# Performance work log

Measured on AMD Instinct MI355X. Metric: run time of the kernel, lower is better.

Reference implementation:

```python
import jax, jax.numpy as jnp
import numpy as np
from jax import lax

EPS = 1e-5

def rmsnorm(x, w, eps=EPS):
    x = jnp.clip(x, -100.0, 100.0)
    var = jnp.clip(jnp.mean(x * x, axis=-1, keepdims=True), eps, None)
    x = jnp.clip(x * lax.rsqrt(var + eps), -10.0, 10.0)
    return w * x

def activation_quant(x):
    x = jnp.clip(x, -50.0, 50.0)
    max_val = jnp.clip(jnp.max(jnp.abs(x), axis=-1, keepdims=True), 0.0001, None)
    scale = 127.0 / max_val
    return jnp.clip(jnp.round(x * scale), -128, 127) / scale

def weight_quant(w):
    scale = jnp.clip(jnp.mean(jnp.abs(w)), 1e-8, None)
    return jnp.sign(w - jnp.mean(w)) * scale

def bitlinear(x, w, norm_w):
    # x: [T, in], w: [out, in], norm_w: [in]
    xn = rmsnorm(x, norm_w)
    xq = xn + lax.stop_gradient(activation_quant(xn) - xn)
    wq = w + lax.stop_gradient(weight_quant(w) - w)
    return jnp.einsum('ti,oi->to', xq, wq)

def expert_fwd(x, wg, wu, wd, n_g, n_u, n_d):
    gate = jnp.clip(bitlinear(x, wg, n_g), -20.0, 20.0)
    up = bitlinear(x, wu, n_u)
    hidden = jnp.clip(jax.nn.silu(gate) * up, -1000.0, 1000.0)
    return bitlinear(hidden, wd, n_d)

def setup_inputs() -> dict:
    key = jax.random.key(0)
    B, S, H, I, E = 4, 2048, 768, 2048, 8
    ks = jax.random.split(key, 12)
    std_h = 0.02 / np.sqrt(H)
    std_i = 0.02 / np.sqrt(I)
    return {
        'hidden_states': jax.random.normal(ks[0], (B, S, H), jnp.float32),
        'router_w': 0.01 * jax.random.normal(ks[1], (E, H), jnp.float32),
        'router_b': jnp.zeros((E,), jnp.float32),
        'Wg': std_h * jax.random.normal(ks[2], (E, I, H), jnp.float32),
        'Wu': std_h * jax.random.normal(ks[3], (E, I, H), jnp.float32),
        'Wd': std_i * jax.random.normal(ks[4], (E, H, I), jnp.float32),
        'ng': jnp.ones((E, H), jnp.float32),
        'nu': jnp.ones((E, H), jnp.float32),
        'nd': jnp.ones((E, I), jnp.float32),
        'sWg': std_h * jax.random.normal(ks[5], (I, H), jnp.float32),
        'sWu': std_h * jax.random.normal(ks[6], (I, H), jnp.float32),
        'sWd': std_i * jax.random.normal(ks[7], (H, I), jnp.float32),
        'sng': jnp.ones((H,), jnp.float32),
        'snu': jnp.ones((H,), jnp.float32),
        'snd': jnp.ones((I,), jnp.float32),
    }

def reference(hidden_states, router_w, router_b, Wg, Wu, Wd, ng, nu, nd, sWg, sWu, sWd, sng, snu, snd):
    B, S, H = hidden_states.shape
    E = router_w.shape[0]
    K = 2  # num_experts_per_tok
    x = hidden_states.reshape(-1, H)  # [T, H]
    router_logits = jnp.einsum('th,eh->te', x, router_w) + router_b  # [T, E]
    routing_weights = jax.nn.softmax(router_logits, axis=-1)
    top_w, top_idx = lax.top_k(routing_weights, K)  # [T, K]
    top_w = top_w / (jnp.sum(top_w, axis=-1, keepdims=True) + 1e-8)
    out = jnp.zeros_like(x)
    for e in range(E):
        w_e = jnp.sum(jnp.where(top_idx == e, top_w, 0.0), axis=-1)  # [T]
        y_e = expert_fwd(x, Wg[e], Wu[e], Wd[e], ng[e], nu[e], nd[e])
        out = out + y_e * w_e[:, None]
    out = out + expert_fwd(x, sWg, sWu, sWd, sng, snu, snd)
    out = jnp.clip(out, -10000.0, 10000.0)
    return out.reshape(B, S, H), router_logits
```

## Files before the change

kernel.cpp:

```cpp
#include <hip/hip_runtime.h>
#include <hip/hip_bf16.h>
#include <math.h>

#define TOK 8192
#define HD 768
#define ID 2048
#define NE 8
#define MSIZE (2048*768)
#define BM 128
#define BK 64
#define R_SHARED 8192
#define R_MAX 25600

typedef int v4i __attribute__((ext_vector_type(4)));
typedef __attribute__((address_space(1))) void gas_void;
typedef __attribute__((address_space(3))) void las_void;

__device__ __forceinline__ void g2lds16(const void* g, void* l) {
  __builtin_amdgcn_global_load_lds((gas_void*)g, (las_void*)l, 16, 0, 0);
}

__device__ __forceinline__ float clipf(float v, float lo, float hi) {
  return fminf(fmaxf(v, lo), hi);
}

__device__ __forceinline__ float wred_sum(float v) {
#pragma unroll
  for (int o = 32; o > 0; o >>= 1) v += __shfl_down(v, o, 64);
  return v;
}
__device__ __forceinline__ float wred_max(float v) {
#pragma unroll
  for (int o = 32; o > 0; o >>= 1) v = fmaxf(v, __shfl_down(v, o, 64));
  return v;
}

__device__ __forceinline__ const float* matsel(int mat, const float* Wg, const float* Wu,
                                               const float* Wd, const float* sWg,
                                               const float* sWu, const float* sWd) {
  if (mat < 8)  return Wg + (size_t)mat * MSIZE;
  if (mat < 16) return Wu + (size_t)(mat - 8) * MSIZE;
  if (mat < 24) return Wd + (size_t)(mat - 16) * MSIZE;
  if (mat == 24) return sWg;
  if (mat == 25) return sWu;
  return sWd;
}

__global__ __launch_bounds__(256)
void k_wstats(const float* __restrict__ Wg, const float* __restrict__ Wu,
              const float* __restrict__ Wd, const float* __restrict__ sWg,
              const float* __restrict__ sWu, const float* __restrict__ sWd,
              double* __restrict__ stats) {
  int mat = blockIdx.y;
  const float* p = matsel(mat, Wg, Wu, Wd, sWg, sWu, sWd);
  int tid = threadIdx.x;
  double s = 0.0, sa = 0.0;
  for (size_t i = (size_t)blockIdx.x * 256 + tid; i < (size_t)MSIZE;
       i += (size_t)gridDim.x * 256) {
    double v = (double)p[i];
    s += v; sa += fabs(v);
  }
  __shared__ double rs[256], ra[256];
  rs[tid] = s; ra[tid] = sa; __syncthreads();
  for (int st = 128; st > 0; st >>= 1) {
    if (tid < st) { rs[tid] += rs[tid + st]; ra[tid] += ra[tid + st]; }
    __syncthreads();
  }
  if (tid == 0) {
    atomicAdd(&stats[mat * 2 + 0], rs[0]);
    atomicAdd(&stats[mat * 2 + 1], ra[0]);
  }
}

__global__ void k_wfinal(const double* __restrict__ stats, double* __restrict__ wmean,
                         float* __restrict__ wscale) {
  int m = threadIdx.x;
  if (m < 27) {
    wmean[m] = stats[m * 2] / (double)MSIZE;
    double sc = stats[m * 2 + 1] / (double)MSIZE;
    wscale[m] = (float)fmax(sc, 1e-8);
  }
}

__global__ __launch_bounds__(256)
void k_wquant(const float* __restrict__ Wg, const float* __restrict__ Wu,
              const float* __restrict__ Wd, const float* __restrict__ sWg,
              const float* __restrict__ sWu, const float* __restrict__ sWd,
              const double* __restrict__ wmean, signed char* __restrict__ tw) {
  int mat = blockIdx.y;
  const float* p = matsel(mat, Wg, Wu, Wd, sWg, sWu, sWd);
  const float4* p4 = (const float4*)p;
  int* t4 = (int*)(tw + (size_t)mat * MSIZE);
  double mu = wmean[mat];
  for (int i = blockIdx.x * 256 + threadIdx.x; i < MSIZE / 4; i += gridDim.x * 256) {
    float4 v = p4[i];
    int b0 = ((double)v.x > mu) ? 1 : (((double)v.x < mu) ? -1 : 0);
    int b1 = ((double)v.y > mu) ? 1 : (((double)v.y < mu) ? -1 : 0);
    int b2 = ((double)v.z > mu) ? 1 : (((double)v.z < mu) ? -1 : 0);
    int b3 = ((double)v.w > mu) ? 1 : (((double)v.w < mu) ? -1 : 0);
    t4[i] = (b0 & 255) | ((b1 & 255) << 8) | ((b2 & 255) << 16) | ((b3 & 255) << 24);
  }
}

__global__ __launch_bounds__(256)
void k_router(const float* __restrict__ x, const float* __restrict__ rw,
              const float* __restrict__ rb, float* __restrict__ logits,
              int* __restrict__ top_idx, float* __restrict__ top_w) {
  int wv = threadIdx.x >> 6, ln = threadIdx.x & 63;
  int t = blockIdx.x * 4 + wv;
  const float4* xr = (const float4*)(x + (size_t)t * HD);
  const float4* rw4 = (const float4*)rw;
  float acc[NE] = {};
#pragma unroll
  for (int i = 0; i < 3; ++i) {
    float4 xv = xr[ln + i * 64];
#pragma unroll
    for (int e = 0; e < NE; ++e) {
      float4 w4 = rw4[e * 192 + ln + i * 64];
      acc[e] += xv.x * w4.x + xv.y * w4.y + xv.z * w4.z + xv.w * w4.w;
    }
  }
#pragma unroll
  for (int e = 0; e < NE; ++e) acc[e] = wred_sum(acc[e]);
  if (ln == 0) {
    float lg[NE], m = -1e30f;
#pragma unroll
    for (int e = 0; e < NE; ++e) {
      lg[e] = acc[e] + rb[e];
      logits[(size_t)t * NE + e] = lg[e];
      m = fmaxf(m, lg[e]);
    }
    float p[NE], s = 0.f;
#pragma unroll
    for (int e = 0; e < NE; ++e) { p[e] = expf(lg[e] - m); s += p[e]; }
    float inv = 1.f / s;
#pragma unroll
    for (int e = 0; e < NE; ++e) p[e] *= inv;
    int e1 = 0; float b1 = p[0];
    for (int e = 1; e < NE; ++e) if (p[e] > b1) { b1 = p[e]; e1 = e; }
    int e2 = -1; float b2 = -1.f;
    for (int e = 0; e < NE; ++e) if (e != e1 && p[e] > b2) { b2 = p[e]; e2 = e; }
    float sw = b1 + b2 + 1e-8f;
    top_idx[t * 2 + 0] = e1; top_idx[t * 2 + 1] = e2;
    top_w[t * 2 + 0] = b1 / sw; top_w[t * 2 + 1] = b2 / sw;
  }
}

__global__ __launch_bounds__(1024)
void k_hist(const int* __restrict__ top_idx, int* __restrict__ counts) {
  __shared__ int h[NE];
  if (threadIdx.x < NE) h[threadIdx.x] = 0;
  __syncthreads();
  for (int i = threadIdx.x; i < TOK * 2; i += 1024) atomicAdd(&h[top_idx[i]], 1);
  __syncthreads();
  if (threadIdx.x < NE) counts[threadIdx.x] = h[threadIdx.x];
}

__global__ void k_initrows(int* __restrict__ rows_token, float* __restrict__ rows_w,
                           int* __restrict__ rows_expert) {
  int r = blockIdx.x * blockDim.x + threadIdx.x;
  if (r >= R_MAX) return;
  if (r < R_SHARED) { rows_token[r] = r; rows_w[r] = 1.f; rows_expert[r] = NE; }
  else { rows_token[r] = -1; rows_w[r] = 0.f; rows_expert[r] = 0; }
}

__global__ void k_offsets(const int* __restrict__ counts, int* __restrict__ offs,
                          int* __restrict__ fill) {
  if (threadIdx.x == 0) {
    int off = R_SHARED;
    for (int e = 0; e < NE; ++e) {
      offs[e] = off;
      off += ((counts[e] + BM - 1) / BM) * BM;
    }
    offs[NE] = off;
  }
  if (threadIdx.x < NE) fill[threadIdx.x] = 0;
}

__global__ __launch_bounds__(256)
void k_scatter(const int* __restrict__ top_idx, const float* __restrict__ top_w,
               const int* __restrict__ offs, int* __restrict__ fill,
               int* __restrict__ rows_token, float* __restrict__ rows_w,
               int* __restrict__ rows_expert, int* __restrict__ inv_row) {
  int t = blockIdx.x * 256 + threadIdx.x;
  int ln = threadIdx.x & 63;
  unsigned long long lt = (ln == 63) ? 0x7fffffffffffffffull
                                     : ((1ull << ln) - 1);
#pragma unroll
  for (int k = 0; k < 2; ++k) {
    int e = top_idx[t * 2 + k];
    unsigned long long peers = 0;
#pragma unroll
    for (int ee = 0; ee < NE; ++ee) {
      unsigned long long m = __ballot(e == ee);
      if (e == ee) peers = m;
    }
    int lead = __ffsll(peers) - 1;
    int rank = __popcll(peers & lt);
    int base = 0;
    if (ln == lead) base = atomicAdd(&fill[e], __popcll(peers));
    base = __shfl(base, lead, 64);
    int r = offs[e] + base + rank;
    rows_token[r] = t;
    rows_w[r] = top_w[t * 2 + k];
    rows_expert[r] = e;
    inv_row[t * 2 + k] = r;
  }
}

__global__ __launch_bounds__(256)
void k_actquant(const float* __restrict__ x, const int* __restrict__ rows_token,
                const int* __restrict__ rows_expert, const float* __restrict__ ng,
                const float* __restrict__ nu, const float* __restrict__ sng,
                const float* __restrict__ snu, signed char* __restrict__ xqg,
                signed char* __restrict__ xqu, float* __restrict__ invg,
                float* __restrict__ invu) {
  int r = blockIdx.x, tid = threadIdx.x;
  int wv = tid >> 6, ln = tid & 63;
  int tok = rows_token[r];
  if (tok < 0) {
    if (tid < 192) {
      ((int*)(xqg + (size_t)r * HD))[tid] = 0;
      ((int*)(xqu + (size_t)r * HD))[tid] = 0;
    }
    if (tid == 0) { invg[r] = 0.f; invu[r] = 0.f; }
    return;
  }
  int e = rows_expert[r];
  const float* wg = (e < NE) ? ng + (size_t)e * HD : sng;
  const float* wu = (e < NE) ? nu + (size_t)e * HD : snu;
  __shared__ float red[3][4];
  float xv[3]; float ss = 0.f;
#pragma unroll
  for (int i = 0; i < 3; ++i) {
    float v = x[(size_t)tok * HD + tid + i * 256];
    v = clipf(v, -100.f, 100.f);
    xv[i] = v; ss += v * v;
  }
  ss = wred_sum(ss);
  if (ln == 0) red[0][wv] = ss;
  __syncthreads();
  float var = fmaxf((red[0][0] + red[0][1] + red[0][2] + red[0][3]) / (float)HD, 1e-5f);
  float rinv = rsqrtf(var + 1e-5f);
  float xng[3], xnu[3]; float ag = 0.f, au = 0.f;
#pragma unroll
  for (int i = 0; i < 3; ++i) {
    float base = clipf(xv[i] * rinv, -10.f, 10.f);
    float tg = clipf(base * wg[tid + i * 256], -50.f, 50.f);
    float tu = clipf(base * wu[tid + i * 256], -50.f, 50.f);
    xng[i] = tg; ag = fmaxf(ag, fabsf(tg));
    xnu[i] = tu; au = fmaxf(au, fabsf(tu));
  }
  ag = wred_max(ag); au = wred_max(au);
  if (ln == 0) { red[1][wv] = ag; red[2][wv] = au; }
  __syncthreads();
  float mg = fmaxf(fmaxf(fmaxf(red[1][0], red[1][1]), fmaxf(red[1][2], red[1][3])), 1e-4f);
  float mu = fmaxf(fmaxf(fmaxf(red[2][0], red[2][1]), fmaxf(red[2][2], red[2][3])), 1e-4f);
  float scg = 127.f / mg, scu = 127.f / mu;
#pragma unroll
  for (int i = 0; i < 3; ++i) {
    xqg[(size_t)r * HD + tid + i * 256] = (signed char)(int)clipf(rintf(xng[i] * scg), -128.f, 127.f);
    xqu[(size_t)r * HD + tid + i * 256] = (signed char)(int)clipf(rintf(xnu[i] * scu), -128.f, 127.f);
  }
  if (tid == 0) { invg[r] = 1.f / scg; invu[r] = 1.f / scu; }
}

__global__ __launch_bounds__(512, 4)
void k_gemm_gu(const signed char* __restrict__ xqg, const signed char* __restrict__ xqu,
               const signed char* __restrict__ tw, const float* __restrict__ wscale,
               const float* __restrict__ invg, const float* __restrict__ invu,
               const int* __restrict__ rows_expert, const int* __restrict__ offs,
               __hip_bfloat16* __restrict__ hidden) {
  int n0 = blockIdx.x * BM;
  int row0 = blockIdx.y * BM;
  if (row0 >= offs[NE]) return;
  int e = rows_expert[row0];
  int mg = (e < NE) ? e : 24;
  int mu = (e < NE) ? e + 8 : 25;
  const signed char* wgp = tw + (size_t)mg * MSIZE;
  const signed char* wup = tw + (size_t)mu * MSIZE;
  __shared__ __align__(16) signed char Ag[2 * BM * BK];
  __shared__ __align__(16) signed char Au[2 * BM * BK];
  __shared__ __align__(16) signed char Bg[2 * BM * BK];
  __shared__ __align__(16) signed char Bu[2 * BM * BK];
  __shared__ float sg[BM], su[BM];
  int tid = threadIdx.x, wv = tid >> 6, ln = tid & 63;
  if (tid < BM) { sg[tid] = invg[row0 + tid]; su[tid] = invu[row0 + tid]; }
  v4i accg[4][2] = {};
  v4i accu[4][2] = {};
  int srow = tid >> 2;
  int swz = (((tid & 3) ^ ((srow >> 1) & 3)) << 4);
  const signed char* pag = xqg + (size_t)(row0 + srow) * HD + swz;
  const signed char* pau = xqu + (size_t)(row0 + srow) * HD + swz;
  const signed char* pbg = wgp + (size_t)(n0 + srow) * HD + swz;
  const signed char* pbu = wup + (size_t)(n0 + srow) * HD + swz;
  int cob = wv * 1024;
  int wm = (wv & 1) * 64, wn = (wv >> 1) * 32;
  int fm = ln & 15;
  int slot16 = (((ln >> 4) ^ ((fm >> 1) & 3)) << 4);
  int offA[4], offB[2];
#pragma unroll
  for (int i = 0; i < 4; ++i) offA[i] = (wm + i * 16 + fm) * BK + slot16;
#pragma unroll
  for (int j = 0; j < 2; ++j) offB[j] = (wn + j * 16 + fm) * BK + slot16;

  auto stage = [&](int buf) {
    int co = buf * 8192 + cob;
    g2lds16(pag, &Ag[co]);
    g2lds16(pau, &Au[co]);
    g2lds16(pbg, &Bg[co]);
    g2lds16(pbu, &Bu[co]);
    pag += BK; pau += BK; pbg += BK; pbu += BK;
  };
  auto compute = [&](int buf) {
    int lb = buf * 8192;
    v4i ar[4], ur[4];
#pragma unroll
    for (int i = 0; i < 4; ++i) {
      ar[i] = *(const v4i*)&Ag[lb + offA[i]];
      ur[i] = *(const v4i*)&Au[lb + offA[i]];
    }
#pragma unroll
    for (int j = 0; j < 2; ++j) {
      v4i bg = *(const v4i*)&Bg[lb + offB[j]];
      v4i bu = *(const v4i*)&Bu[lb + offB[j]];
#pragma unroll
      for (int i = 0; i < 4; ++i) {
        accg[i][j] = __builtin_amdgcn_mfma_i32_16x16x64_i8(ar[i], bg, accg[i][j], 0, 0, 0);
        accu[i][j] = __builtin_amdgcn_mfma_i32_16x16x64_i8(ur[i], bu, accu[i][j], 0, 0, 0);
      }
    }
  };

  const int NIT = HD / BK;
  stage(0);
#pragma unroll 1
  for (int it = 0; it < NIT; it += 2) {
    __syncthreads();
    if (it + 1 < NIT) stage(1);
    compute(0);
    __syncthreads();
    if (it + 2 < NIT) stage(0);
    compute(1);
  }

  float gs = wscale[mg], us = wscale[mu];
  int dq = (ln >> 4) * 4, dn = ln & 15;
#pragma unroll
  for (int i = 0; i < 4; ++i) {
#pragma unroll
    for (int rg = 0; rg < 4; ++rg) {
      int lrow = wm + i * 16 + dq + rg;
      int grow = row0 + lrow;
      float ig = gs * sg[lrow];
      float iu = us * su[lrow];
#pragma unroll
      for (int j = 0; j < 2; ++j) {
        int gcol = n0 + wn + j * 16 + dn;
        float g = (float)accg[i][j][rg] * ig;
        g = clipf(g, -20.f, 20.f);
        float sil = g * __builtin_amdgcn_rcpf(1.f + __expf(-g));
        float u = (float)accu[i][j][rg] * iu;
        float h = clipf(sil * u, -1000.f, 1000.f);
        hidden[(size_t)grow * ID + gcol] = __float2bfloat16(h);
      }
    }
  }
}

__global__ __launch_bounds__(256)
void k_hquant(const __hip_bfloat16* __restrict__ hidden, const int* __restrict__ rows_token,
              const int* __restrict__ rows_expert, const float* __restrict__ nd,
              const float* __restrict__ snd, signed char* __restrict__ hq,
              float* __restrict__ invh) {
  int r = blockIdx.x, tid = threadIdx.x;
  int wv = tid >> 6, ln = tid & 63;
  int tok = rows_token[r];
  if (tok < 0) {
    ((unsigned long long*)(hq + (size_t)r * ID))[tid] = 0ull;
    if (tid == 0) invh[r] = 0.f;
    return;
  }
  int e = rows_expert[r];
  const float2* wn2 = (const float2*)((e < NE) ? nd + (size_t)e * ID : snd);
  const unsigned int* h2 = (const unsigned int*)(hidden + (size_t)r * ID);
  __shared__ float red[2][4];
  float xa[4], xb[4]; float ss = 0.f;
#pragma unroll
  for (int i = 0; i < 4; ++i) {
    unsigned int u = h2[tid + i * 256];
    float a = __uint_as_float(u << 16);
    float b = __uint_as_float(u & 0xffff0000u);
    a = clipf(a, -100.f, 100.f); b = clipf(b, -100.f, 100.f);
    xa[i] = a; xb[i] = b; ss += a * a + b * b;
  }
  ss = wred_sum(ss);
  if (ln == 0) red[0][wv] = ss;
  __syncthreads();
  float var = fmaxf((red[0][0] + red[0][1] + red[0][2] + red[0][3]) / (float)ID, 1e-5f);
  float rinv = rsqrtf(var + 1e-5f);
  float na[4], nb[4]; float amax = 0.f;
#pragma unroll
  for (int i = 0; i < 4; ++i) {
    float2 w = wn2[tid + i * 256];
    float ta = clipf(clipf(xa[i] * rinv, -10.f, 10.f) * w.x, -50.f, 50.f);
    float tb = clipf(clipf(xb[i] * rinv, -10.f, 10.f) * w.y, -50.f, 50.f);
    na[i] = ta; nb[i] = tb;
    amax = fmaxf(amax, fmaxf(fabsf(ta), fabsf(tb)));
  }
  amax = wred_max(amax);
  if (ln == 0) red[1][wv] = amax;
  __syncthreads();
  float mx = fmaxf(fmaxf(fmaxf(red[1][0], red[1][1]), fmaxf(red[1][2], red[1][3])), 1e-4f);
  float sc = 127.f / mx;
  unsigned short* hqs = (unsigned short*)(hq + (size_t)r * ID);
#pragma unroll
  for (int i = 0; i < 4; ++i) {
    int qa = (int)clipf(rintf(na[i] * sc), -128.f, 127.f);
    int qb = (int)clipf(rintf(nb[i] * sc), -128.f, 127.f);
    hqs[tid + i * 256] = (unsigned short)((qa & 255) | ((qb & 255) << 8));
  }
  if (tid == 0) invh[r] = 1.f / sc;
}

__global__ __launch_bounds__(512, 4)
void k_gemm_down(const signed char* __restrict__ hq, const signed char* __restrict__ tw,
                 const float* __restrict__ wscale, const float* __restrict__ invh,
                 const float* __restrict__ rows_w, const int* __restrict__ rows_expert,
                 const int* __restrict__ offs, float* __restrict__ y) {
  int n0 = blockIdx.x * BM;
  int row0 = blockIdx.y * BM;
  if (row0 >= offs[NE]) return;
  int e = rows_expert[row0];
  int md = (e < NE) ? 16 + e : 26;
  const signed char* wdp = tw + (size_t)md * MSIZE;
  __shared__ __align__(16) signed char As[2 * BM * BK];
  __shared__ __align__(16) signed char Bs[2 * BM * BK];
  __shared__ float s_f[BM];
  int tid = threadIdx.x, wv = tid >> 6, ln = tid & 63;
  if (tid < BM) s_f[tid] = invh[row0 + tid] * rows_w[row0 + tid];
  v4i acc[4][2] = {};
  int srow = tid >> 2;
  int swz = (((tid & 3) ^ ((srow >> 1) & 3)) << 4);
  const signed char* pa = hq + (size_t)(row0 + srow) * ID + swz;
  const signed char* pb = wdp + (size_t)(n0 + srow) * ID + swz;
  int cob = wv * 1024;
  int wm = (wv & 1) * 64, wn = (wv >> 1) * 32;
  int fm = ln & 15;
  int slot16 = (((ln >> 4) ^ ((fm >> 1) & 3)) << 4);
  int offA[4], offB[2];
#pragma unroll
  for (int i = 0; i < 4; ++i) offA[i] = (wm + i * 16 + fm) * BK + slot16;
#pragma unroll
  for (int j = 0; j < 2; ++j) offB[j] = (wn + j * 16 + fm) * BK + slot16;

  auto stage = [&](int buf) {
    int co = buf * 8192 + cob;
    g2lds16(pa, &As[co]);
    g2lds16(pb, &Bs[co]);
    pa += BK; pb += BK;
  };
  auto compute = [&](int buf) {
    int lb = buf * 8192;
    v4i a[4];
#pragma unroll
    for (int i = 0; i < 4; ++i) a[i] = *(const v4i*)&As[lb + offA[i]];
#pragma unroll
    for (int j = 0; j < 2; ++j) {
      v4i b = *(const v4i*)&Bs[lb + offB[j]];
#pragma unroll
      for (int i = 0; i < 4; ++i)
        acc[i][j] = __builtin_amdgcn_mfma_i32_16x16x64_i8(a[i], b, acc[i][j], 0, 0, 0);
    }
  };

  const int NIT = ID / BK;
  stage(0);
#pragma unroll 1
  for (int it = 0; it < NIT; it += 2) {
    __syncthreads();
    if (it + 1 < NIT) stage(1);
    compute(0);
    __syncthreads();
    if (it + 2 < NIT) stage(0);
    compute(1);
  }

  float ds = wscale[md];
  int dq = (ln >> 4) * 4, dn = ln & 15;
#pragma unroll
  for (int i = 0; i < 4; ++i) {
#pragma unroll
    for (int rg = 0; rg < 4; ++rg) {
      int lrow = wm + i * 16 + dq + rg;
      float f = ds * s_f[lrow];
#pragma unroll
      for (int j = 0; j < 2; ++j) {
        int gcol = n0 + wn + j * 16 + dn;
        y[(size_t)(row0 + lrow) * HD + gcol] = (float)acc[i][j][rg] * f;
      }
    }
  }
}

__global__ __launch_bounds__(192)
void k_gather(const float* __restrict__ y, const int* __restrict__ inv_row,
              float* __restrict__ out) {
  int t = blockIdx.x, c = threadIdx.x;
  int r1 = inv_row[t * 2 + 0], r2 = inv_row[t * 2 + 1];
  const float4* y4 = (const float4*)y;
  float4 a = y4[(size_t)t * 192 + c];
  float4 b = y4[(size_t)r1 * 192 + c];
  float4 d = y4[(size_t)r2 * 192 + c];
  float4 o;
  o.x = clipf(a.x + b.x + d.x, -10000.f, 10000.f);
  o.y = clipf(a.y + b.y + d.y, -10000.f, 10000.f);
  o.z = clipf(a.z + b.z + d.z, -10000.f, 10000.f);
  o.w = clipf(a.w + b.w + d.w, -10000.f, 10000.f);
  ((float4*)out)[(size_t)t * 192 + c] = o;
}

extern "C" void kernel_launch(void* const* d_in, const int* in_sizes, int n_in,
                              void* d_out, int out_size, void* d_ws, size_t ws_size,
                              hipStream_t stream) {
  (void)in_sizes; (void)n_in; (void)out_size; (void)ws_size;
  const float* x   = (const float*)d_in[0];
  const float* rw  = (const float*)d_in[1];
  const float* rb  = (const float*)d_in[2];
  const float* Wg  = (const float*)d_in[3];
  const float* Wu  = (const float*)d_in[4];
  const float* Wd  = (const float*)d_in[5];
  const float* ng  = (const float*)d_in[6];
  const float* nu  = (const float*)d_in[7];
  const float* nd  = (const float*)d_in[8];
  const float* sWg = (const float*)d_in[9];
  const float* sWu = (const float*)d_in[10];
  const float* sWd = (const float*)d_in[11];
  const float* sng = (const float*)d_in[12];
  const float* snu = (const float*)d_in[13];
  const float* snd = (const float*)d_in[14];
  float* out = (float*)d_out;
  float* logits = out + (size_t)TOK * HD;

  char* ws = (char*)d_ws;
  size_t off = 0;
  auto alloc = [&](size_t b) { size_t o = off; off = (off + b + 255) & ~(size_t)255; return o; };
  signed char* tw   = (signed char*)(ws + alloc((size_t)27 * MSIZE));
  double* stats     = (double*)(ws + alloc(27 * 2 * sizeof(double)));
  double* wmean     = (double*)(ws + alloc(27 * sizeof(double)));
  float* wscale     = (float*)(ws + alloc(27 * sizeof(float)));
  int* counts       = (int*)(ws + alloc(8 * sizeof(int)));
  int* fill         = (int*)(ws + alloc(8 * sizeof(int)));
  int* offs         = (int*)(ws + alloc(16 * sizeof(int)));
  int* top_idx      = (int*)(ws + alloc((size_t)TOK * 2 * sizeof(int)));
  float* top_w      = (float*)(ws + alloc((size_t)TOK * 2 * sizeof(float)));
  int* inv_row      = (int*)(ws + alloc((size_t)TOK * 2 * sizeof(int)));
  int* rows_token   = (int*)(ws + alloc((size_t)R_MAX * sizeof(int)));
  float* rows_w     = (float*)(ws + alloc((size_t)R_MAX * sizeof(float)));
  int* rows_expert  = (int*)(ws + alloc((size_t)R_MAX * sizeof(int)));
  float* invg       = (float*)(ws + alloc((size_t)R_MAX * sizeof(float)));
  float* invu       = (float*)(ws + alloc((size_t)R_MAX * sizeof(float)));
  float* invh       = (float*)(ws + alloc((size_t)R_MAX * sizeof(float)));
  signed char* hq   = (signed char*)(ws + alloc((size_t)R_MAX * ID));
  signed char* xqg  = hq;
  signed char* xqu  = hq + (size_t)R_MAX * HD;
  char* hid_region  = ws + alloc((size_t)R_MAX * ID * 2);
  __hip_bfloat16* hidden = (__hip_bfloat16*)hid_region;
  float* y          = (float*)hid_region;

  hipMemsetAsync(stats, 0, 27 * 2 * sizeof(double), stream);

  k_wstats<<<dim3(64, 27), 256, 0, stream>>>(Wg, Wu, Wd, sWg, sWu, sWd, stats);
  k_wfinal<<<1, 32, 0, stream>>>(stats, wmean, wscale);
  k_wquant<<<dim3(256, 27), 256, 0, stream>>>(Wg, Wu, Wd, sWg, sWu, sWd, wmean, tw);
  k_router<<<TOK / 4, 256, 0, stream>>>(x, rw, rb, logits, top_idx, top_w);
  k_hist<<<1, 1024, 0, stream>>>(top_idx, counts);
  k_initrows<<<(R_MAX + 255) / 256, 256, 0, stream>>>(rows_token, rows_w, rows_expert);
  k_offsets<<<1, 64, 0, stream>>>(counts, offs, fill);
  k_scatter<<<TOK / 256, 256, 0, stream>>>(top_idx, top_w, offs, fill, rows_token,
                                           rows_w, rows_expert, inv_row);
  k_actquant<<<R_MAX, 256, 0, stream>>>(x, rows_token, rows_expert, ng, nu, sng, snu,
                                        xqg, xqu, invg, invu);
  k_gemm_gu<<<dim3(ID / BM, R_MAX / BM), 512, 0, stream>>>(xqg, xqu, tw, wscale, invg, invu,
                                                           rows_expert, offs, hidden);
  k_hquant<<<R_MAX, 256, 0, stream>>>(hidden, rows_token, rows_expert, nd, snd, hq, invh);
  k_gemm_down<<<dim3(HD / BM, R_MAX / BM), 512, 0, stream>>>(hq, tw, wscale, invh,
                                                             rows_w, rows_expert, offs, y);
  k_gather<<<TOK, 192, 0, stream>>>(y, inv_row, out);
}
```

Before: 598.7 us.

## Split gate/up GEMM and switch to 32x32x32 MFMA with direct-global B loads

Replaces the fused gate+up GEMM with two separate kernels sharing a new gemm_core that uses 32x32x32 int8 MFMA, 256-thread blocks, and loads the weight (B) operand directly from global memory into registers instead of staging it through LDS. The gate kernel writes clipped gate values as bf16 into the hidden buffer, and the up kernel reads them back to apply SiLU and the product. The down GEMM is moved onto the same core. This cuts LDS footprint and instruction count per MFMA, but adds an extra bf16 write and read of the full hidden buffer plus uncoalesced, unstaged global B loads.

Measured after the change: 770.5 us. 28.7% more time.

```diff
diff --git a/kernel.cpp b/kernel.cpp
--- a/kernel.cpp
+++ b/kernel.cpp
@@ -13,6 +13,7 @@
 #define R_MAX 25600
 
 typedef int v4i __attribute__((ext_vector_type(4)));
+typedef int v16i __attribute__((ext_vector_type(16)));
 typedef __attribute__((address_space(1))) void gas_void;
 typedef __attribute__((address_space(3))) void las_void;
 
@@ -265,107 +266,135 @@
   if (tid == 0) { invg[r] = 1.f / scg; invu[r] = 1.f / scu; }
 }
 
-__global__ __launch_bounds__(512, 4)
-void k_gemm_gu(const signed char* __restrict__ xqg, const signed char* __restrict__ xqu,
-               const signed char* __restrict__ tw, const float* __restrict__ wscale,
-               const float* __restrict__ invg, const float* __restrict__ invu,
-               const int* __restrict__ rows_expert, const int* __restrict__ offs,
-               __hip_bfloat16* __restrict__ hidden) {
-  int n0 = blockIdx.x * BM;
-  int row0 = blockIdx.y * BM;
+__device__ __forceinline__ void gemm_core(const signed char* __restrict__ aq,
+                                          const signed char* __restrict__ bp,
+                                          int row0, int n0, int kdim, int nit,
+                                          signed char* As, v16i acc[2][2]) {
+  int tid = threadIdx.x, wv = tid >> 6, ln = tid & 63;
+  int lr = ln & 31, lh = ln >> 5;
+  const signed char* pa[2];
+#pragma unroll
+  for (int j = 0; j < 2; ++j)
+    pa[j] = aq + (size_t)(row0 + wv * 32 + lr) * kdim + j * 32 + lh * 16;
+  const signed char* pb[2];
+#pragma unroll
+  for (int j = 0; j < 2; ++j)
+    pb[j] = bp + (size_t)(n0 + (wv >> 1) * 64 + j * 32 + lr) * kdim + lh * 16;
+  int offA[2][2];
+#pragma unroll
+  for (int i = 0; i < 2; ++i)
+#pragma unroll
+    for (int kc = 0; kc < 2; ++kc)
+      offA[i][kc] = ((((wv & 1) * 2 + i) * 2 + kc) << 10) + ln * 16;
+
+  auto stage = [&](int buf) {
+#pragma unroll
+    for (int j = 0; j < 2; ++j) {
+      g2lds16(pa[j], As + buf * 8192 + ((wv * 2 + j) << 10));
+      pa[j] += BK;
+    }
+  };
+  auto compute = [&](int buf) {
+    v4i b[2][2];
+#pragma unroll
+    for (int j = 0; j < 2; ++j) {
+      b[j][0] = *(const v4i*)(pb[j]);
+      b[j][1] = *(const v4i*)(pb[j] + 32);
+      pb[j] += BK;
+    }
+    v4i a[2][2];
+#pragma unroll
+    for (int i = 0; i < 2; ++i)
+#pragma unroll
+      for (int kc = 0; kc < 2; ++kc)
+        a[i][kc] = *(const v4i*)(As + buf * 8192 + offA[i][kc]);
+#pragma unroll
+    for (int kc = 0; kc < 2; ++kc)
+#pragma unroll
+      for (int i = 0; i < 2; ++i)
+#pragma unroll
+        for (int j = 0; j < 2; ++j)
+          acc[i][j] = __builtin_amdgcn_mfma_i32_32x32x32_i8(a[i][kc], b[j][kc], acc[i][j], 0, 0, 0);
+  };
+
+  stage(0);
+#pragma unroll 1
+  for (int it = 0; it < nit; it += 2) {
+    __syncthreads();
+    if (it + 1 < nit) stage(1);
+    compute(0);
+    __syncthreads();
+    if (it + 2 < nit) stage(0);
+    compute(1);
+  }
+}
+
+
+__global__ __launch_bounds__(256, 3)
+void k_gemm_gate(const signed char* __restrict__ xq, const signed char* __restrict__ tw,
+                 const float* __restrict__ wscale, const float* __restrict__ invx,
+                 const int* __restrict__ rows_expert, const int* __restrict__ offs,
+                 __hip_bfloat16* __restrict__ gbuf) {
+  int n0 = blockIdx.x * BM, row0 = blockIdx.y * BM;
   if (row0 >= offs[NE]) return;
   int e = rows_expert[row0];
   int mg = (e < NE) ? e : 24;
+  __shared__ __align__(16) signed char As[2 * 8192];
+  __shared__ float sx[BM];
+  if (threadIdx.x < BM) sx[threadIdx.x] = invx[row0 + threadIdx.x];
+  v16i acc[2][2] = {};
+  gemm_core(xq, tw + (size_t)mg * MSIZE, row0, n0, HD, HD / BK, As, acc);
+  float ws = wscale[mg];
+  int wv = threadIdx.x >> 6, ln = threadIdx.x & 63;
+  int wm = (wv & 1) * 64, wn = (wv >> 1) * 64;
+  int lr = ln & 31, lh = ln >> 5;
+#pragma unroll
+  for (int i = 0; i < 2; ++i)
+#pragma unroll
+    for (int j = 0; j < 2; ++j)
+#pragma unroll
+      for (int r = 0; r < 16; ++r) {
+        int row = wm + i * 32 + (r & 3) + 8 * (r >> 2) + 4 * lh;
+        int col = n0 + wn + j * 32 + lr;
+        float g = (float)acc[i][j][r] * ws * sx[row];
+        g = clipf(g, -20.f, 20.f);
+        gbuf[(size_t)(row0 + row) * ID + col] = __float2bfloat16(g);
+      }
+}
+
+__global__ __launch_bounds__(256, 3)
+void k_gemm_up(const signed char* __restrict__ xq, const signed char* __restrict__ tw,
+               const float* __restrict__ wscale, const float* __restrict__ invx,
+               const int* __restrict__ rows_expert, const int* __restrict__ offs,
+               __hip_bfloat16* __restrict__ gbuf) {
+  int n0 = blockIdx.x * BM, row0 = blockIdx.y * BM;
+  if (row0 >= offs[NE]) return;
+  int e = rows_expert[row0];
   int mu = (e < NE) ? e + 8 : 25;
-  const signed char* wgp = tw + (size_t)mg * MSIZE;
-  const signed char* wup = tw + (size_t)mu * MSIZE;
-  __shared__ __align__(16) signed char Ag[2 * BM * BK];
-  __shared__ __align__(16) signed char Au[2 * BM * BK];
-  __shared__ __align__(16) signed char Bg[2 * BM * BK];
-  __shared__ __align__(16) signed char Bu[2 * BM * BK];
-  __shared__ float sg[BM], su[BM];
-  int tid = threadIdx.x, wv = tid >> 6, ln = tid & 63;
-  if (tid < BM) { sg[tid] = invg[row0 + tid]; su[tid] = invu[row0 + tid]; }
-  v4i accg[4][2] = {};
-  v4i accu[4][2] = {};
-  int srow = tid >> 2;
-  int swz = (((tid & 3) ^ ((srow >> 1) & 3)) << 4);
-  const signed char* pag = xqg + (size_t)(row0 + srow) * HD + swz;
-  const signed char* pau = xqu + (size_t)(row0 + srow) * HD + swz;
-  const signed char* pbg = wgp + (size_t)(n0 + srow) * HD + swz;
-  const signed char* pbu = wup + (size_t)(n0 + srow) * HD + swz;
-  int cob = wv * 1024;
-  int wm = (wv & 1) * 64, wn = (wv >> 1) * 32;
-  int fm = ln & 15;
-  int slot16 = (((ln >> 4) ^ ((fm >> 1) & 3)) << 4);
-  int offA[4], offB[2];
-#pragma unroll
-  for (int i = 0; i < 4; ++i) offA[i] = (wm + i * 16 + fm) * BK + slot16;
-#pragma unroll
-  for (int j = 0; j < 2; ++j) offB[j] = (wn + j * 16 + fm) * BK + slot16;
-
-  auto stage = [&](int buf) {
-    int co = buf * 8192 + cob;
-    g2lds16(pag, &Ag[co]);
-    g2lds16(pau, &Au[co]);
-    g2lds16(pbg, &Bg[co]);
-    g2lds16(pbu, &Bu[co]);
-    pag += BK; pau += BK; pbg += BK; pbu += BK;
-  };
-  auto compute = [&](int buf) {
-    int lb = buf * 8192;
-    v4i ar[4], ur[4];
-#pragma unroll
-    for (int i = 0; i < 4; ++i) {
-      ar[i] = *(const v4i*)&Ag[lb + offA[i]];
-      ur[i] = *(const v4i*)&Au[lb + offA[i]];
-    }
-#pragma unroll
-    for (int j = 0; j < 2; ++j) {
-      v4i bg = *(const v4i*)&Bg[lb + offB[j]];
-      v4i bu = *(const v4i*)&Bu[lb + offB[j]];
-#pragma unroll
-      for (int i = 0; i < 4; ++i) {
-        accg[i][j] = __builtin_amdgcn_mfma_i32_16x16x64_i8(ar[i], bg, accg[i][j], 0, 0, 0);
-        accu[i][j] = __builtin_amdgcn_mfma_i32_16x16x64_i8(ur[i], bu, accu[i][j], 0, 0, 0);
+  __shared__ __align__(16) signed char As[2 * 8192];
+  __shared__ float sx[BM];
+  if (threadIdx.x < BM) sx[threadIdx.x] = invx[row0 + threadIdx.x];
+  v16i acc[2][2] = {};
+  gemm_core(xq, tw + (size_t)mu * MSIZE, row0, n0, HD, HD / BK, As, acc);
+  float ws = wscale[mu];
+  int wv = threadIdx.x >> 6, ln = threadIdx.x & 63;
+  int wm = (wv & 1) * 64, wn = (wv >> 1) * 64;
+  int lr = ln & 31, lh = ln >> 5;
+#pragma unroll
+  for (int i = 0; i < 2; ++i)
+#pragma unroll
+    for (int j = 0; j < 2; ++j)
+#pragma unroll
+      for (int r = 0; r < 16; ++r) {
+        int row = wm + i * 32 + (r & 3) + 8 * (r >> 2) + 4 * lh;
+        int col = n0 + wn + j * 32 + lr;
+        size_t idx = (size_t)(row0 + row) * ID + col;
+        float u = (float)acc[i][j][r] * ws * sx[row];
+        float gf = __bfloat162float(gbuf[idx]);
+        float sil = gf * __builtin_amdgcn_rcpf(1.f + __expf(-gf));
+        float h = clipf(sil * u, -1000.f, 1000.f);
+        gbuf[idx] = __float2bfloat16(h);
       }
-    }
-  };
-
-  const int NIT = HD / BK;
-  stage(0);
-#pragma unroll 1
-  for (int it = 0; it < NIT; it += 2) {
-    __syncthreads();
-    if (it + 1 < NIT) stage(1);
-    compute(0);
-    __syncthreads();
-    if (it + 2 < NIT) stage(0);
-    compute(1);
-  }
-
-  float gs = wscale[mg], us = wscale[mu];
-  int dq = (ln >> 4) * 4, dn = ln & 15;
-#pragma unroll
-  for (int i = 0; i < 4; ++i) {
-#pragma unroll
-    for (int rg = 0; rg < 4; ++rg) {
-      int lrow = wm + i * 16 + dq + rg;
-      int grow = row0 + lrow;
-      float ig = gs * sg[lrow];
-      float iu = us * su[lrow];
-#pragma unroll
-      for (int j = 0; j < 2; ++j) {
-        int gcol = n0 + wn + j * 16 + dn;
-        float g = (float)accg[i][j][rg] * ig;
-        g = clipf(g, -20.f, 20.f);
-        float sil = g * __builtin_amdgcn_rcpf(1.f + __expf(-g));
-        float u = (float)accu[i][j][rg] * iu;
-        float h = clipf(sil * u, -1000.f, 1000.f);
-        hidden[(size_t)grow * ID + gcol] = __float2bfloat16(h);
-      }
-    }
-  }
 }
 
 __global__ __launch_bounds__(256)
@@ -423,84 +452,35 @@
   if (tid == 0) invh[r] = 1.f / sc;
 }
 
-__global__ __launch_bounds__(512, 4)
+__global__ __launch_bounds__(256, 3)
 void k_gemm_down(const signed char* __restrict__ hq, const signed char* __restrict__ tw,
                  const float* __restrict__ wscale, const float* __restrict__ invh,
                  const float* __restrict__ rows_w, const int* __restrict__ rows_expert,
                  const int* __restrict__ offs, float* __restrict__ y) {
-  int n0 = blockIdx.x * BM;
-  int row0 = blockIdx.y * BM;
+  int n0 = blockIdx.x * BM, row0 = blockIdx.y * BM;
   if (row0 >= offs[NE]) return;
   int e = rows_expert[row0];
   int md = (e < NE) ? 16 + e : 26;
-  const signed char* wdp = tw + (size_t)md * MSIZE;
-  __shared__ __align__(16) signed char As[2 * BM * BK];
-  __shared__ __align__(16) signed char Bs[2 * BM * BK];
+  __shared__ __align__(16) signed char As[2 * 8192];
   __shared__ float s_f[BM];
-  int tid = threadIdx.x, wv = tid >> 6, ln = tid & 63;
-  if (tid < BM) s_f[tid] = invh[row0 + tid] * rows_w[row0 + tid];
-  v4i acc[4][2] = {};
-  int srow = tid >> 2;
-  int swz = (((tid & 3) ^ ((srow >> 1) & 3)) << 4);
-  const signed char* pa = hq + (size_t)(row0 + srow) * ID + swz;
-  const signed char* pb = wdp + (size_t)(n0 + srow) * ID + swz;
-  int cob = wv * 1024;
-  int wm = (wv & 1) * 64, wn = (wv >> 1) * 32;
-  int fm = ln & 15;
-  int slot16 = (((ln >> 4) ^ ((fm >> 1) & 3)) << 4);
-  int offA[4], offB[2];
-#pragma unroll
-  for (int i = 0; i < 4; ++i) offA[i] = (wm + i * 16 + fm) * BK + slot16;
-#pragma unroll
-  for (int j = 0; j < 2; ++j) offB[j] = (wn + j * 16 + fm) * BK + slot16;
-
-  auto stage = [&](int buf) {
-    int co = buf * 8192 + cob;
-    g2lds16(pa, &As[co]);
-    g2lds16(pb, &Bs[co]);
-    pa += BK; pb += BK;
-  };
-  auto compute = [&](int buf) {
-    int lb = buf * 8192;
-    v4i a[4];
-#pragma unroll
-    for (int i = 0; i < 4; ++i) a[i] = *(const v4i*)&As[lb + offA[i]];
-#pragma unroll
-    for (int j = 0; j < 2; ++j) {
-      v4i b = *(const v4i*)&Bs[lb + offB[j]];
-#pragma unroll
-      for (int i = 0; i < 4; ++i)
-        acc[i][j] = __builtin_amdgcn_mfma_i32_16x16x64_i8(a[i], b, acc[i][j], 0, 0, 0);
-    }
-  };
-
-  const int NIT = ID / BK;
-  stage(0);
-#pragma unroll 1
-  for (int it = 0; it < NIT; it += 2) {
-    __syncthreads();
-    if (it + 1 < NIT) stage(1);
-    compute(0);
-    __syncthreads();
-    if (it + 2 < NIT) stage(0);
-    compute(1);
-  }
-
-  float ds = wscale[md];
-  int dq = (ln >> 4) * 4, dn = ln & 15;
-#pragma unroll
-  for (int i = 0; i < 4; ++i) {
-#pragma unroll
-    for (int rg = 0; rg < 4; ++rg) {
-      int lrow = wm + i * 16 + dq + rg;
-      float f = ds * s_f[lrow];
-#pragma unroll
-      for (int j = 0; j < 2; ++j) {
-        int gcol = n0 + wn + j * 16 + dn;
-        y[(size_t)(row0 + lrow) * HD + gcol] = (float)acc[i][j][rg] * f;
+  if (threadIdx.x < BM)
+    s_f[threadIdx.x] = invh[row0 + threadIdx.x] * rows_w[row0 + threadIdx.x];
+  v16i acc[2][2] = {};
+  gemm_core(hq, tw + (size_t)md * MSIZE, row0, n0, ID, ID / BK, As, acc);
+  float ws = wscale[md];
+  int wv = threadIdx.x >> 6, ln = threadIdx.x & 63;
+  int wm = (wv & 1) * 64, wn = (wv >> 1) * 64;
+  int lr = ln & 31, lh = ln >> 5;
+#pragma unroll
+  for (int i = 0; i < 2; ++i)
+#pragma unroll
+    for (int j = 0; j < 2; ++j)
+#pragma unroll
+      for (int r = 0; r < 16; ++r) {
+        int row = wm + i * 32 + (r & 3) + 8 * (r >> 2) + 4 * lh;
+        int col = n0 + wn + j * 32 + lr;
+        y[(size_t)(row0 + row) * HD + col] = (float)acc[i][j][r] * ws * s_f[row];
       }
-    }
-  }
 }
 
 __global__ __launch_bounds__(192)
@@ -581,10 +561,12 @@
                                            rows_w, rows_expert, inv_row);
   k_actquant<<<R_MAX, 256, 0, stream>>>(x, rows_token, rows_expert, ng, nu, sng, snu,
                                         xqg, xqu, invg, invu);
-  k_gemm_gu<<<dim3(ID / BM, R_MAX / BM), 512, 0, stream>>>(xqg, xqu, tw, wscale, invg, invu,
+  k_gemm_gate<<<dim3(ID / BM, R_MAX / BM), 256, 0, stream>>>(xqg, tw, wscale, invg,
+                                                             rows_expert, offs, hidden);
+  k_gemm_up<<<dim3(ID / BM, R_MAX / BM), 256, 0, stream>>>(xqu, tw, wscale, invu,
                                                            rows_expert, offs, hidden);
   k_hquant<<<R_MAX, 256, 0, stream>>>(hidden, rows_token, rows_expert, nd, snd, hq, invh);
-  k_gemm_down<<<dim3(HD / BM, R_MAX / BM), 512, 0, stream>>>(hq, tw, wscale, invh,
+  k_gemm_down<<<dim3(HD / BM, R_MAX / BM), 256, 0, stream>>>(hq, tw, wscale, invh,
                                                              rows_w, rows_expert, offs, y);
   k_gather<<<TOK, 192, 0, stream>>>(y, inv_row, out);
 }
```

## Switch int8 GEMMs to 32x32x32 MFMA with wave-split gate/up

Applied to the files above, without the earlier changes.

Both expert GEMMs move from 16x16x64 int8 MFMA to 32x32x32 int8 MFMA, with a new LDS layout in which each 1 KB chunk holds a 32-row by 32-byte fragment that can be read linearly per lane. In the gate/up kernel, half the waves now compute gate and half compute up, instead of every wave doing both. The gate results are exchanged through LDS so the SiLU*up epilogue can be fused, at the cost of an extra LDS round trip and two barriers. The down GEMM drops to 256 threads per block, with each thread staging two chunks. The aim is higher MFMA efficiency and fewer LDS fragment reads per MAC, though the non-coalesced epilogue stores and the LDS exchange could offset it.

Result: slower. 698.6 us (+16.7%).

```diff
diff --git a/kernel.cpp b/kernel.cpp
--- a/kernel.cpp
+++ b/kernel.cpp
@@ -8,11 +8,11 @@
 #define NE 8
 #define MSIZE (2048*768)
 #define BM 128
-#define BK 64
 #define R_SHARED 8192
 #define R_MAX 25600
 
 typedef int v4i __attribute__((ext_vector_type(4)));
+typedef int v16i __attribute__((ext_vector_type(16)));
 typedef __attribute__((address_space(1))) void gas_void;
 typedef __attribute__((address_space(3))) void las_void;
 
@@ -279,60 +279,50 @@
   int mu = (e < NE) ? e + 8 : 25;
   const signed char* wgp = tw + (size_t)mg * MSIZE;
   const signed char* wup = tw + (size_t)mu * MSIZE;
-  __shared__ __align__(16) signed char Ag[2 * BM * BK];
-  __shared__ __align__(16) signed char Au[2 * BM * BK];
-  __shared__ __align__(16) signed char Bg[2 * BM * BK];
-  __shared__ __align__(16) signed char Bu[2 * BM * BK];
+  __shared__ __align__(16) char smem[65536];
+  signed char* Ag = (signed char*)smem;
+  signed char* Au = Ag + 16384;
+  signed char* Bg = Au + 16384;
+  signed char* Bu = Bg + 16384;
   __shared__ float sg[BM], su[BM];
   int tid = threadIdx.x, wv = tid >> 6, ln = tid & 63;
-  if (tid < BM) { sg[tid] = invg[row0 + tid]; su[tid] = invu[row0 + tid]; }
-  v4i accg[4][2] = {};
-  v4i accu[4][2] = {};
-  int srow = tid >> 2;
-  int swz = (((tid & 3) ^ ((srow >> 1) & 3)) << 4);
-  const signed char* pag = xqg + (size_t)(row0 + srow) * HD + swz;
-  const signed char* pau = xqu + (size_t)(row0 + srow) * HD + swz;
-  const signed char* pbg = wgp + (size_t)(n0 + srow) * HD + swz;
-  const signed char* pbu = wup + (size_t)(n0 + srow) * HD + swz;
-  int cob = wv * 1024;
-  int wm = (wv & 1) * 64, wn = (wv >> 1) * 32;
-  int fm = ln & 15;
-  int slot16 = (((ln >> 4) ^ ((fm >> 1) & 3)) << 4);
-  int offA[4], offB[2];
-#pragma unroll
-  for (int i = 0; i < 4; ++i) offA[i] = (wm + i * 16 + fm) * BK + slot16;
-#pragma unroll
-  for (int j = 0; j < 2; ++j) offB[j] = (wn + j * 16 + fm) * BK + slot16;
+  int lr = ln & 31, lh = ln >> 5;
+  if (tid < BM) { sg[tid] = invg[tid + row0]; su[tid] = invu[tid + row0]; }
+  int skc = wv >> 2, smt = wv & 3;
+  const signed char* pag = xqg + (size_t)(row0 + smt * 32 + lr) * HD + skc * 32 + lh * 16;
+  const signed char* pau = xqu + (size_t)(row0 + smt * 32 + lr) * HD + skc * 32 + lh * 16;
+  const signed char* pbg = wgp + (size_t)(n0 + smt * 32 + lr) * HD + skc * 32 + lh * 16;
+  const signed char* pbu = wup + (size_t)(n0 + smt * 32 + lr) * HD + skc * 32 + lh * 16;
+  int ldst = wv * 1024;
+  int isUp = wv >> 2, q = wv & 3;
+  const signed char* Ax = isUp ? Au : Ag;
+  const signed char* Bx = isUp ? Bu : Bg;
+  int am0 = (q & 1) * 2, bn0 = (q >> 1) * 2;
+  v16i acc[2][2] = {};
 
   auto stage = [&](int buf) {
-    int co = buf * 8192 + cob;
-    g2lds16(pag, &Ag[co]);
-    g2lds16(pau, &Au[co]);
-    g2lds16(pbg, &Bg[co]);
-    g2lds16(pbu, &Bu[co]);
-    pag += BK; pau += BK; pbg += BK; pbu += BK;
+    g2lds16(pag, Ag + buf * 8192 + ldst);
+    g2lds16(pau, Au + buf * 8192 + ldst);
+    g2lds16(pbg, Bg + buf * 8192 + ldst);
+    g2lds16(pbu, Bu + buf * 8192 + ldst);
+    pag += 64; pau += 64; pbg += 64; pbu += 64;
   };
   auto compute = [&](int buf) {
-    int lb = buf * 8192;
-    v4i ar[4], ur[4];
-#pragma unroll
-    for (int i = 0; i < 4; ++i) {
-      ar[i] = *(const v4i*)&Ag[lb + offA[i]];
-      ur[i] = *(const v4i*)&Au[lb + offA[i]];
-    }
-#pragma unroll
-    for (int j = 0; j < 2; ++j) {
-      v4i bg = *(const v4i*)&Bg[lb + offB[j]];
-      v4i bu = *(const v4i*)&Bu[lb + offB[j]];
-#pragma unroll
-      for (int i = 0; i < 4; ++i) {
-        accg[i][j] = __builtin_amdgcn_mfma_i32_16x16x64_i8(ar[i], bg, accg[i][j], 0, 0, 0);
-        accu[i][j] = __builtin_amdgcn_mfma_i32_16x16x64_i8(ur[i], bu, accu[i][j], 0, 0, 0);
-      }
+    int lb = buf * 8192 + ln * 16;
+#pragma unroll
+    for (int kc = 0; kc < 2; ++kc) {
+      v4i a0 = *(const v4i*)(Ax + lb + ((kc * 4 + am0) << 10));
+      v4i a1 = *(const v4i*)(Ax + lb + ((kc * 4 + am0 + 1) << 10));
+      v4i b0 = *(const v4i*)(Bx + lb + ((kc * 4 + bn0) << 10));
+      v4i b1 = *(const v4i*)(Bx + lb + ((kc * 4 + bn0 + 1) << 10));
+      acc[0][0] = __builtin_amdgcn_mfma_i32_32x32x32_i8(a0, b0, acc[0][0], 0, 0, 0);
+      acc[0][1] = __builtin_amdgcn_mfma_i32_32x32x32_i8(a0, b1, acc[0][1], 0, 0, 0);
+      acc[1][0] = __builtin_amdgcn_mfma_i32_32x32x32_i8(a1, b0, acc[1][0], 0, 0, 0);
+      acc[1][1] = __builtin_amdgcn_mfma_i32_32x32x32_i8(a1, b1, acc[1][1], 0, 0, 0);
     }
   };
 
-  const int NIT = HD / BK;
+  const int NIT = HD / 64;
   stage(0);
 #pragma unroll 1
   for (int it = 0; it < NIT; it += 2) {
@@ -344,27 +334,40 @@
     compute(1);
   }
 
-  float gs = wscale[mg], us = wscale[mu];
-  int dq = (ln >> 4) * 4, dn = ln & 15;
-#pragma unroll
-  for (int i = 0; i < 4; ++i) {
-#pragma unroll
-    for (int rg = 0; rg < 4; ++rg) {
-      int lrow = wm + i * 16 + dq + rg;
-      int grow = row0 + lrow;
-      float ig = gs * sg[lrow];
-      float iu = us * su[lrow];
-#pragma unroll
-      for (int j = 0; j < 2; ++j) {
-        int gcol = n0 + wn + j * 16 + dn;
-        float g = (float)accg[i][j][rg] * ig;
-        g = clipf(g, -20.f, 20.f);
-        float sil = g * __builtin_amdgcn_rcpf(1.f + __expf(-g));
-        float u = (float)accu[i][j][rg] * iu;
-        float h = clipf(sil * u, -1000.f, 1000.f);
-        hidden[(size_t)grow * ID + gcol] = __float2bfloat16(h);
-      }
-    }
+  __syncthreads();
+  float* gls = (float*)smem;
+  int wm = am0 * 32, wn = bn0 * 32;
+  if (!isUp) {
+    float gs = wscale[mg];
+#pragma unroll
+    for (int mt = 0; mt < 2; ++mt)
+#pragma unroll
+      for (int nt = 0; nt < 2; ++nt)
+#pragma unroll
+        for (int r = 0; r < 16; ++r) {
+          int row = wm + mt * 32 + (r & 3) + 8 * (r >> 2) + 4 * lh;
+          int col = wn + nt * 32 + lr;
+          float g = (float)acc[mt][nt][r] * gs * sg[row];
+          gls[row * BM + col] = clipf(g, -20.f, 20.f);
+        }
+  }
+  __syncthreads();
+  if (isUp) {
+    float us = wscale[mu];
+#pragma unroll
+    for (int mt = 0; mt < 2; ++mt)
+#pragma unroll
+      for (int nt = 0; nt < 2; ++nt)
+#pragma unroll
+        for (int r = 0; r < 16; ++r) {
+          int row = wm + mt * 32 + (r & 3) + 8 * (r >> 2) + 4 * lh;
+          int col = wn + nt * 32 + lr;
+          float u = (float)acc[mt][nt][r] * us * su[row];
+          float gf = gls[row * BM + col];
+          float sil = gf * __builtin_amdgcn_rcpf(1.f + __expf(-gf));
+          float h = clipf(sil * u, -1000.f, 1000.f);
+          hidden[(size_t)(row0 + row) * ID + n0 + col] = __float2bfloat16(h);
+        }
   }
 }
 
@@ -423,7 +426,7 @@
   if (tid == 0) invh[r] = 1.f / sc;
 }
 
-__global__ __launch_bounds__(512, 4)
+__global__ __launch_bounds__(256, 4)
 void k_gemm_down(const signed char* __restrict__ hq, const signed char* __restrict__ tw,
                  const float* __restrict__ wscale, const float* __restrict__ invh,
                  const float* __restrict__ rows_w, const int* __restrict__ rows_expert,
@@ -434,47 +437,49 @@
   int e = rows_expert[row0];
   int md = (e < NE) ? 16 + e : 26;
   const signed char* wdp = tw + (size_t)md * MSIZE;
-  __shared__ __align__(16) signed char As[2 * BM * BK];
-  __shared__ __align__(16) signed char Bs[2 * BM * BK];
+  __shared__ __align__(16) signed char As[2 * 8192];
+  __shared__ __align__(16) signed char Bs[2 * 8192];
   __shared__ float s_f[BM];
   int tid = threadIdx.x, wv = tid >> 6, ln = tid & 63;
+  int lr = ln & 31, lh = ln >> 5;
   if (tid < BM) s_f[tid] = invh[row0 + tid] * rows_w[row0 + tid];
-  v4i acc[4][2] = {};
-  int srow = tid >> 2;
-  int swz = (((tid & 3) ^ ((srow >> 1) & 3)) << 4);
-  const signed char* pa = hq + (size_t)(row0 + srow) * ID + swz;
-  const signed char* pb = wdp + (size_t)(n0 + srow) * ID + swz;
-  int cob = wv * 1024;
-  int wm = (wv & 1) * 64, wn = (wv >> 1) * 32;
-  int fm = ln & 15;
-  int slot16 = (((ln >> 4) ^ ((fm >> 1) & 3)) << 4);
-  int offA[4], offB[2];
-#pragma unroll
-  for (int i = 0; i < 4; ++i) offA[i] = (wm + i * 16 + fm) * BK + slot16;
-#pragma unroll
-  for (int j = 0; j < 2; ++j) offB[j] = (wn + j * 16 + fm) * BK + slot16;
+  const signed char* pa[2]; const signed char* pb[2];
+  int ldst[2];
+#pragma unroll
+  for (int j = 0; j < 2; ++j) {
+    int idx = wv * 2 + j;
+    int kc = idx >> 2, mt = idx & 3;
+    pa[j] = hq + (size_t)(row0 + mt * 32 + lr) * ID + kc * 32 + lh * 16;
+    pb[j] = wdp + (size_t)(n0 + mt * 32 + lr) * ID + kc * 32 + lh * 16;
+    ldst[j] = idx * 1024;
+  }
+  int am0 = (wv & 1) * 2, bn0 = (wv >> 1) * 2;
+  v16i acc[2][2] = {};
 
   auto stage = [&](int buf) {
-    int co = buf * 8192 + cob;
-    g2lds16(pa, &As[co]);
-    g2lds16(pb, &Bs[co]);
-    pa += BK; pb += BK;
+#pragma unroll
+    for (int j = 0; j < 2; ++j) {
+      g2lds16(pa[j], As + buf * 8192 + ldst[j]);
+      g2lds16(pb[j], Bs + buf * 8192 + ldst[j]);
+      pa[j] += 64; pb[j] += 64;
+    }
   };
   auto compute = [&](int buf) {
-    int lb = buf * 8192;
-    v4i a[4];
-#pragma unroll
-    for (int i = 0; i < 4; ++i) a[i] = *(const v4i*)&As[lb + offA[i]];
-#pragma unroll
-    for (int j = 0; j < 2; ++j) {
-      v4i b = *(const v4i*)&Bs[lb + offB[j]];
-#pragma unroll
-      for (int i = 0; i < 4; ++i)
-        acc[i][j] = __builtin_amdgcn_mfma_i32_16x16x64_i8(a[i], b, acc[i][j], 0, 0, 0);
+    int lb = buf * 8192 + ln * 16;
+#pragma unroll
+    for (int kc = 0; kc < 2; ++kc) {
+      v4i a0 = *(const v4i*)(As + lb + ((kc * 4 + am0) << 10));
+      v4i a1 = *(const v4i*)(As + lb + ((kc * 4 + am0 + 1) << 10));
+      v4i b0 = *(const v4i*)(Bs + lb + ((kc * 4 + bn0) << 10));
+      v4i b1 = *(const v4i*)(Bs + lb + ((kc * 4 + bn0 + 1) << 10));
+      acc[0][0] = __builtin_amdgcn_mfma_i32_32x32x32_i8(a0, b0, acc[0][0], 0, 0, 0);
+      acc[0][1] = __builtin_amdgcn_mfma_i32_32x32x32_i8(a0, b1, acc[0][1], 0, 0, 0);
+      acc[1][0] = __builtin_amdgcn_mfma_i32_32x32x32_i8(a1, b0, acc[1][0], 0, 0, 0);
+      acc[1][1] = __builtin_amdgcn_mfma_i32_32x32x32_i8(a1, b1, acc[1][1], 0, 0, 0);
     }
   };
 
-  const int NIT = ID / BK;
+  const int NIT = ID / 64;
   stage(0);
 #pragma unroll 1
   for (int it = 0; it < NIT; it += 2) {
@@ -487,20 +492,17 @@
   }
 
   float ds = wscale[md];
-  int dq = (ln >> 4) * 4, dn = ln & 15;
-#pragma unroll
-  for (int i = 0; i < 4; ++i) {
-#pragma unroll
-    for (int rg = 0; rg < 4; ++rg) {
-      int lrow = wm + i * 16 + dq + rg;
-      float f = ds * s_f[lrow];
-#pragma unroll
-      for (int j = 0; j < 2; ++j) {
-        int gcol = n0 + wn + j * 16 + dn;
-        y[(size_t)(row0 + lrow) * HD + gcol] = (float)acc[i][j][rg] * f;
+  int wm = am0 * 32, wn = bn0 * 32;
+#pragma unroll
+  for (int mt = 0; mt < 2; ++mt)
+#pragma unroll
+    for (int nt = 0; nt < 2; ++nt)
+#pragma unroll
+      for (int r = 0; r < 16; ++r) {
+        int row = wm + mt * 32 + (r & 3) + 8 * (r >> 2) + 4 * lh;
+        int col = n0 + wn + nt * 32 + lr;
+        y[(size_t)(row0 + row) * HD + col] = (float)acc[mt][nt][r] * ds * s_f[row];
       }
-    }
-  }
 }
 
 __global__ __launch_bounds__(192)
@@ -584,7 +586,7 @@
   k_gemm_gu<<<dim3(ID / BM, R_MAX / BM), 512, 0, stream>>>(xqg, xqu, tw, wscale, invg, invu,
                                                            rows_expert, offs, hidden);
   k_hquant<<<R_MAX, 256, 0, stream>>>(hidden, rows_token, rows_expert, nd, snd, hq, invh);
-  k_gemm_down<<<dim3(HD / BM, R_MAX / BM), 512, 0, stream>>>(hq, tw, wscale, invh,
+  k_gemm_down<<<dim3(HD / BM, R_MAX / BM), 256, 0, stream>>>(hq, tw, wscale, invh,
                                                              rows_w, rows_expert, offs, y);
   k_gather<<<TOK, 192, 0, stream>>>(y, inv_row, out);
 }
```
